# Performance work log

Measured on AMD Instinct MI355X. Metric: run time of the kernel, lower is better.

Reference implementation:

```python
import jax, jax.numpy as jnp
import numpy as np

# ---- module hyperparameters (match init_kwargs) ----
DIM = 512
HEADS = 8
KEY_DIM = 32
ATTN_RATIO = 4
D = ATTN_RATIO * KEY_DIM          # 128, per-head value dim
RES = 28                          # H = W = resolution
B = 64
KS = 5                            # depthwise conv kernel
EPS = 1e-5
SCALE = KEY_DIM ** (-0.5)


def bn(x, p):
    """Inference-mode BatchNorm2d. x: [B,C,H,W], p: [4,C] = (gamma, beta, mean, var)."""
    g, b, m, v = p
    inv = g * jax.lax.rsqrt(v + EPS)
    return x * inv[None, :, None, None] + (b - m * inv)[None, :, None, None]


def conv1x1(x, w):
    """1x1 conv as channel GEMM. x: [B,C,H,W], w: [O,C] -> [B,O,H,W]."""
    return jnp.einsum('oc,bchw->bohw', w, x)


def setup_inputs() -> dict:
    key = jax.random.key(0)
    ks = jax.random.split(key, 12)

    def bnp(k, c):
        k1, k2, k3, k4 = jax.random.split(k, 4)
        return jnp.stack([
            jax.random.uniform(k1, (c,), minval=0.5, maxval=1.5),   # gamma
            jax.random.normal(k2, (c,)) * 0.1,                       # beta
            jax.random.normal(k3, (c,)) * 0.1,                       # running mean
            jax.random.uniform(k4, (c,), minval=0.5, maxval=1.5),   # running var
        ])

    x = jax.random.normal(ks[0], (B, DIM, RES, RES), dtype=jnp.float32)
    qk_w = jax.random.normal(ks[1], (DIM // 2, DIM)) * 0.05
    qk_bn = bnp(ks[2], DIM // 2)
    dws_w = jax.random.normal(ks[3], (DIM // 4, 1, KS, KS)) * 0.05   # depthwise OIHW, I=1
    dws_bn = bnp(ks[4], DIM // 4)
    vs_w = jax.random.normal(ks[5], (HEADS, D, DIM // HEADS)) * 0.05
    vs_bn = jnp.stack([bnp(jax.random.fold_in(ks[6], i), D) for i in range(HEADS)])
    proj_w = jax.random.normal(ks[7], (DIM, D * HEADS)) * 0.05
    proj_bn = bnp(ks[8], DIM)
    # relative-position bias tables over offsets 0..RES-1 (offset -> its own index)
    bias_h = jax.random.normal(ks[9], (1, RES)) * 0.02
    bias_w = jax.random.normal(ks[10], (1, RES)) * 0.02
    bias_idx = jnp.asarray(np.abs(np.arange(RES)[:, None] - np.arange(RES)[None, :]), jnp.int32)
    return dict(x=x, qk_w=qk_w, qk_bn=qk_bn, dws_w=dws_w, dws_bn=dws_bn,
                vs_w=vs_w, vs_bn=vs_bn, proj_w=proj_w, proj_bn=proj_bn,
                bias_h=bias_h, bias_w=bias_w, bias_idx=bias_idx)


def reference(x, qk_w, qk_bn, dws_w, dws_bn, vs_w, vs_bn, proj_w, proj_bn,
              bias_h, bias_w, bias_idx):
    # gathered relative-position biases, [RES, RES]
    ab_h = bias_h[0][bias_idx]
    ab_w = bias_w[0][bias_idx]

    feat = bn(conv1x1(x, qk_w), qk_bn)            # [B, DIM/2, H, W]
    q, k = jnp.split(feat, 2, axis=1)             # each [B, DIM/4, H, W]
    q = bn(jax.lax.conv_general_dilated(
        q, dws_w, (1, 1), 'SAME',
        dimension_numbers=('NCHW', 'OIHW', 'NCHW'),
        feature_group_count=DIM // 4), dws_bn)

    qr_w = q.transpose(0, 2, 3, 1)                # [B, H, W, C4]
    kr_w = k.transpose(0, 2, 3, 1)
    attn_w = jax.nn.softmax(
        jnp.einsum('bhqc,bhkc->bhqk', qr_w, kr_w) * SCALE + ab_w, axis=-1)  # [B,H,W,W]

    qr_h = qr_w.transpose(0, 2, 1, 3)             # [B, W, H, C4]
    kr_h = kr_w.transpose(0, 2, 1, 3)
    attn_h = jax.nn.softmax(
        jnp.einsum('bwqc,bwkc->bwqk', qr_h, kr_h) * SCALE + ab_h, axis=-1)  # [B,W,H,H]

    feats_in = jnp.split(x, HEADS, axis=1)        # each [B, DIM/HEADS, H, W]
    feats_out = []
    feat = feats_in[0]
    for i in range(HEADS):                        # sequential cascade over heads
        if i > 0:
            feat = feat + feats_in[i]
        v = bn(conv1x1(feat, vs_w[i]), vs_bn[i]).transpose(0, 2, 3, 1)  # [B,H,W,D]
        v = jnp.einsum('bhqk,bhkd->bhqd', attn_w, v)                    # row attention
        v = v.transpose(0, 2, 1, 3)                                     # [B,W,H,D]
        f = jnp.einsum('bwqk,bwkd->bwqd', attn_h, v)                    # col attention
        feats_out.append(f.transpose(0, 3, 2, 1))                       # [B,D,H,W]

    out = jnp.concatenate(feats_out, axis=1)      # [B, D*HEADS, H, W]
    out = bn(conv1x1(jax.nn.relu(out), proj_w), proj_bn)                # [B,DIM,H,W]
    return out
```

## Files before the change

kernel.cpp:

```cpp
#include <hip/hip_runtime.h>
#include <hip/hip_fp16.h>

#define NB 64
#define NSP 784
#define CDIM 512
#define CQK 256
#define C4 128
#define NHEADS 8
#define CCAT 1024
#define BN_EPS 1e-5f
#define ATT_SCALE 0.17677669529663687f

using half8_t = __attribute__((ext_vector_type(8))) _Float16;
using half4_t = __attribute__((ext_vector_type(4))) _Float16;
using half2_t = __attribute__((ext_vector_type(2))) _Float16;
using f32x4_t = __attribute__((ext_vector_type(4))) float;

__device__ __forceinline__ void bn_coef(const float* bn, int cout, int o, float& inv, float& add) {
    float g = bn[o], be = bn[cout + o], m = bn[2 * cout + o], v = bn[3 * cout + o];
    inv = g * rsqrtf(v + BN_EPS);
    add = be - m * inv;
}

__device__ __forceinline__ float fdot2(half2_t a, half2_t b, float c) {
#if __has_builtin(__builtin_amdgcn_fdot2)
    return __builtin_amdgcn_fdot2(a, b, c, false);
#else
    return c + (float)a[0] * (float)b[0] + (float)a[1] * (float)b[1];
#endif
}

__device__ __forceinline__ void gload16(const void* g, void* l) {
    __builtin_amdgcn_global_load_lds(
        (const __attribute__((address_space(1))) void*)g,
        (__attribute__((address_space(3))) void*)l, 16, 0, 0);
}

__global__ __launch_bounds__(256)
void transpose_x_kernel(const float* __restrict__ x, _Float16* __restrict__ xt)
{
    __shared__ _Float16 t[32 * 786];
    const int b = blockIdx.y, c0 = blockIdx.x * 32;
    const float* src = x + ((long)b * CDIM + c0) * NSP;
    for (int i = threadIdx.x; i < 32 * NSP; i += 256) {
        const int c = i / NSP, sp = i - c * NSP;
        t[c * 786 + sp] = (_Float16)src[i];
    }
    __syncthreads();
    _Float16* dst = xt + (long)b * NSP * CDIM + c0;
    for (int sp = threadIdx.x; sp < NSP; sp += 256) {
        half8_t* d8 = (half8_t*)(dst + (long)sp * CDIM);
#pragma unroll
        for (int q = 0; q < 4; ++q) {
            half8_t v;
#pragma unroll
            for (int j = 0; j < 8; ++j) v[j] = t[(q * 8 + j) * 786 + sp];
            d8[q] = v;
        }
    }
}

__global__ __launch_bounds__(256)
void convert_w_kernel(const float* __restrict__ qk, const float* __restrict__ vs,
                      const float* __restrict__ pj, _Float16* __restrict__ dst)
{
    const int e = (blockIdx.x * 256 + threadIdx.x) * 4;
    const float* src; int off; _Float16* d;
    if (e < 131072)      { src = qk; off = e;          d = dst; }
    else if (e < 196608) { src = vs; off = e - 131072; d = dst + 131072; }
    else                 { src = pj; off = e - 196608; d = dst + 196608; }
    const float4 v = *(const float4*)(src + off);
    half4_t h; h[0] = (_Float16)v.x; h[1] = (_Float16)v.y; h[2] = (_Float16)v.z; h[3] = (_Float16)v.w;
    *(half4_t*)(d + off) = h;
}

template<int CIN, int NT, bool OUT_T>
__global__ __launch_bounds__(256)
void mfma_gemm_kernel(const _Float16* __restrict__ inH, const _Float16* __restrict__ wA,
                      const float* __restrict__ bnp, void* __restrict__ outp, int cout)
{
    __shared__ _Float16 As[8192];
    __shared__ _Float16 Bs[8192];
    const int tid = threadIdx.x;
    const int lane = tid & 63;
    const int wv = tid >> 6;
    const int wm = wv >> 1, wn = wv & 1;
    const int grp = gridDim.x >> 3;
    const int tile = (blockIdx.x & 7) * grp + (blockIdx.x >> 3);
    const int oBase = (tile % NT) * 128;
    const int colBase = (tile / NT) * 128;

    f32x4_t acc[4][4];
#pragma unroll
    for (int i = 0; i < 4; ++i)
#pragma unroll
        for (int j = 0; j < 4; ++j) acc[i][j] = (f32x4_t){0.f, 0.f, 0.f, 0.f};

    for (int k0 = 0; k0 < CIN; k0 += 64) {
        if (k0) __syncthreads();
#pragma unroll
        for (int it = 0; it < 4; ++it) {
            const int s = it * 256 + tid;
            const int sidx = s >> 3;
            const int skg = (s & 7) ^ (sidx & 7);
            gload16(wA + (long)(oBase + sidx) * CIN + k0 + skg * 8, As + s * 8);
            gload16(inH + (long)(colBase + sidx) * CIN + k0 + skg * 8, Bs + s * 8);
        }
        __syncthreads();
#pragma unroll
        for (int ks = 0; ks < 2; ++ks) {
            const int kq = ks * 4 + (lane >> 4);
            half8_t a[4], b[4];
#pragma unroll
            for (int mf = 0; mf < 4; ++mf) {
                const int idx = wm * 64 + mf * 16 + (lane & 15);
                a[mf] = *(const half8_t*)(As + (idx * 8 + (kq ^ (idx & 7))) * 8);
            }
#pragma unroll
            for (int nf = 0; nf < 4; ++nf) {
                const int idx = wn * 64 + nf * 16 + (lane & 15);
                b[nf] = *(const half8_t*)(Bs + (idx * 8 + (kq ^ (idx & 7))) * 8);
            }
#pragma unroll
            for (int mf = 0; mf < 4; ++mf)
#pragma unroll
                for (int nf = 0; nf < 4; ++nf)
                    acc[mf][nf] = __builtin_amdgcn_mfma_f32_16x16x32_f16(a[mf], b[nf], acc[mf][nf], 0, 0, 0);
        }
    }

    const int rbase = wm * 64 + (lane >> 4) * 4;
    const int cbase = colBase + wn * 64 + (lane & 15);
#pragma unroll
    for (int mf = 0; mf < 4; ++mf) {
        const int o0 = oBase + rbase + mf * 16;
        float inv[4], add[4];
#pragma unroll
        for (int j = 0; j < 4; ++j) bn_coef(bnp, cout, o0 + j, inv[j], add[j]);
#pragma unroll
        for (int nf = 0; nf < 4; ++nf) {
            const int col = cbase + nf * 16;
            if constexpr (OUT_T) {
                _Float16* dst = (_Float16*)outp + (long)col * cout + o0;
                half4_t v;
#pragma unroll
                for (int j = 0; j < 4; ++j) v[j] = (_Float16)(acc[mf][nf][j] * inv[j] + add[j]);
                *(half4_t*)dst = v;
            } else {
                const int bb = col / NSP, sp = col - bb * NSP;
                float* dst = (float*)outp + ((long)bb * cout + o0) * NSP + sp;
#pragma unroll
                for (int j = 0; j < 4; ++j) dst[(long)j * NSP] = acc[mf][nf][j] * inv[j] + add[j];
            }
        }
    }
}

__global__ __launch_bounds__(256)
void vall_kernel(const _Float16* __restrict__ xt, const _Float16* __restrict__ vsw,
                 const float* __restrict__ vsbn, _Float16* __restrict__ concat_t)
{
    __shared__ _Float16 As[8192];
    __shared__ _Float16 Bs[8192];
    const int tid = threadIdx.x, lane = tid & 63;
    const int wv = tid >> 6, wm = wv >> 1, wn = wv & 1;
    const int colBase = blockIdx.x * 128;

    float bacc[4][8];
#pragma unroll
    for (int it = 0; it < 4; ++it)
#pragma unroll
        for (int j = 0; j < 8; ++j) bacc[it][j] = 0.f;

    for (int head = 0; head < NHEADS; ++head) {
        if (head) __syncthreads();
#pragma unroll
        for (int it = 0; it < 4; ++it) {
            const int c = it * 256 + tid;
            const int kg = c & 7, idx = c >> 3;
            const half8_t xv = *(const half8_t*)(xt + (long)(colBase + idx) * CDIM + head * 64 + kg * 8);
            half8_t bv;
#pragma unroll
            for (int j = 0; j < 8; ++j) { bacc[it][j] += (float)xv[j]; bv[j] = (_Float16)bacc[it][j]; }
            *(half8_t*)(Bs + (idx * 8 + (kg ^ (idx & 7))) * 8) = bv;
            const int skg = kg ^ (idx & 7);
            gload16(vsw + (long)head * (C4 * 64) + idx * 64 + skg * 8, As + c * 8);
        }
        __syncthreads();

        f32x4_t acc[4][4];
#pragma unroll
        for (int i = 0; i < 4; ++i)
#pragma unroll
            for (int j = 0; j < 4; ++j) acc[i][j] = (f32x4_t){0.f, 0.f, 0.f, 0.f};
#pragma unroll
        for (int ks = 0; ks < 2; ++ks) {
            const int kq = ks * 4 + (lane >> 4);
            half8_t a[4], b[4];
#pragma unroll
            for (int mf = 0; mf < 4; ++mf) {
                const int idx = wm * 64 + mf * 16 + (lane & 15);
                a[mf] = *(const half8_t*)(As + (idx * 8 + (kq ^ (idx & 7))) * 8);
            }
#pragma unroll
            for (int nf = 0; nf < 4; ++nf) {
                const int idx = wn * 64 + nf * 16 + (lane & 15);
                b[nf] = *(const half8_t*)(Bs + (idx * 8 + (kq ^ (idx & 7))) * 8);
            }
#pragma unroll
            for (int mf = 0; mf < 4; ++mf)
#pragma unroll
                for (int nf = 0; nf < 4; ++nf)
                    acc[mf][nf] = __builtin_amdgcn_mfma_f32_16x16x32_f16(a[mf], b[nf], acc[mf][nf], 0, 0, 0);
        }

        const int rbase = wm * 64 + (lane >> 4) * 4;
        const int cbase = colBase + wn * 64 + (lane & 15);
        const float* bnh = vsbn + head * 4 * C4;
#pragma unroll
        for (int mf = 0; mf < 4; ++mf) {
            const int o0 = rbase + mf * 16;
            float inv[4], add[4];
#pragma unroll
            for (int j = 0; j < 4; ++j) bn_coef(bnh, C4, o0 + j, inv[j], add[j]);
#pragma unroll
            for (int nf = 0; nf < 4; ++nf) {
                const int col = cbase + nf * 16;
                _Float16* dst = concat_t + (long)col * CCAT + head * C4 + o0;
                half4_t v;
#pragma unroll
                for (int j = 0; j < 4; ++j) v[j] = (_Float16)(acc[mf][nf][j] * inv[j] + add[j]);
                *(half4_t*)dst = v;
            }
        }
    }
}

__global__ __launch_bounds__(256)
void dwconv_t_kernel(const _Float16* __restrict__ feat_t, const float* __restrict__ dww,
                     const float* __restrict__ dwbn, _Float16* __restrict__ qdw_t)
{
    const int h = blockIdx.x, b = blockIdx.y, ch0 = blockIdx.z * 64;
    __shared__ _Float16 rows[5][32][64];
    for (int i = threadIdx.x; i < 5 * 32 * 64; i += 256) {
        const int dy = i / (32 * 64);
        const int rem = i - dy * (32 * 64);
        const int iw = rem >> 6, c = rem & 63;
        const int ih = h + dy - 2, w = iw - 2;
        _Float16 v = (_Float16)0.f;
        if (ih >= 0 && ih < 28 && w >= 0 && w < 28)
            v = feat_t[((long)b * NSP + ih * 28 + w) * CQK + ch0 + c];
        rows[dy][iw][c] = v;
    }
    const int pr = threadIdx.x & 31;
    const int c2 = pr * 2;
    float wr0[25], wr1[25];
#pragma unroll
    for (int q = 0; q < 25; ++q) {
        wr0[q] = dww[(ch0 + c2) * 25 + q];
        wr1[q] = dww[(ch0 + c2 + 1) * 25 + q];
    }
    float inv0, add0, inv1, add1;
    bn_coef(dwbn, C4, ch0 + c2, inv0, add0);
    bn_coef(dwbn, C4, ch0 + c2 + 1, inv1, add1);
    __syncthreads();
    for (int l = threadIdx.x; l < 28 * 32; l += 256) {
        const int w = l >> 5;
        float a0 = 0.f, a1 = 0.f;
#pragma unroll
        for (int dy = 0; dy < 5; ++dy)
#pragma unroll
            for (int dx = 0; dx < 5; ++dx) {
                const half2_t v2 = *(const half2_t*)(&rows[dy][w + dx][c2]);
                a0 += wr0[dy * 5 + dx] * (float)v2[0];
                a1 += wr1[dy * 5 + dx] * (float)v2[1];
            }
        half2_t o2; o2[0] = (_Float16)(a0 * inv0 + add0); o2[1] = (_Float16)(a1 * inv1 + add1);
        *(half2_t*)(qdw_t + ((long)b * NSP + h * 28 + w) * C4 + ch0 + c2) = o2;
    }
}

template<bool ROWMODE>
__global__ __launch_bounds__(256)
void attn_map_kernel(const _Float16* __restrict__ qdw_t, const _Float16* __restrict__ feat_t,
                     const float* __restrict__ biasv, _Float16* __restrict__ attn_out)
{
    const int fix = blockIdx.x, b = blockIdx.y;
    __shared__ _Float16 Qs[28][136];
    __shared__ _Float16 Ks[28][136];
    __shared__ float S[28][28];
    __shared__ float bsh[28];
    if (threadIdx.x < 28) bsh[threadIdx.x] = biasv[threadIdx.x];
    for (int l = threadIdx.x; l < 28 * 16; l += 256) {
        const int p = l >> 4, c8 = (l & 15) * 8;
        const int sp = ROWMODE ? (fix * 28 + p) : (p * 28 + fix);
        *(half8_t*)(&Qs[p][c8]) = *(const half8_t*)(qdw_t + ((long)b * NSP + sp) * C4 + c8);
        *(half8_t*)(&Ks[p][c8]) = *(const half8_t*)(feat_t + ((long)b * NSP + sp) * CQK + 128 + c8);
    }
    __syncthreads();
    for (int e = threadIdx.x; e < 784; e += 256) {
        const int qp = e / 28, kp = e - (e / 28) * 28;
        float acc = 0.f;
        const half2_t* qv = (const half2_t*)&Qs[qp][0];
        const half2_t* kv = (const half2_t*)&Ks[kp][0];
#pragma unroll
        for (int c = 0; c < 64; ++c) acc = fdot2(qv[c], kv[c], acc);
        const int dd = qp - kp;
        S[qp][kp] = acc * ATT_SCALE + bsh[dd < 0 ? -dd : dd];
    }
    __syncthreads();
    const int r = threadIdx.x >> 3, g = threadIdx.x & 7;
    if (r < 28) {
        float mx = -1e30f;
#pragma unroll
        for (int j = 0; j < 4; ++j) { const int k = g + j * 8; if (k < 28) mx = fmaxf(mx, S[r][k]); }
        mx = fmaxf(mx, __shfl_xor(mx, 1));
        mx = fmaxf(mx, __shfl_xor(mx, 2));
        mx = fmaxf(mx, __shfl_xor(mx, 4));
        float e4[4], sum = 0.f;
#pragma unroll
        for (int j = 0; j < 4; ++j) {
            const int k = g + j * 8;
            e4[j] = (k < 28) ? __expf(S[r][k] - mx) : 0.f;
            sum += e4[j];
        }
        sum += __shfl_xor(sum, 1);
        sum += __shfl_xor(sum, 2);
        sum += __shfl_xor(sum, 4);
        const float rinv = 1.f / sum;
#pragma unroll
        for (int j = 0; j < 4; ++j) { const int k = g + j * 8; if (k < 28) S[r][k] = e4[j] * rinv; }
    }
    __syncthreads();
    _Float16* dst = attn_out + ((long)b * 28 + fix) * 1024;
    for (int i = threadIdx.x; i < 1024; i += 256) {
        const int q = i >> 5, k = i & 31;
        dst[i] = (q < 28 && k < 28) ? (_Float16)S[q][k] : (_Float16)0.f;
    }
}

__global__ __launch_bounds__(512)
void fused_stage_kernel(_Float16* __restrict__ concat_t,
                        const _Float16* __restrict__ attw,
                        const _Float16* __restrict__ atth)
{
    const int wgid = ((int)blockIdx.x & 7) * ((int)gridDim.x >> 3) + ((int)blockIdx.x >> 3);
    const int b = wgid >> 6, dq = wgid & 63;
    __shared__ _Float16 V[16 * 906];
    __shared__ _Float16 M1[28 * 17 * 42];
    const int tid = threadIdx.x, lane = tid & 63, wv = tid >> 6;
    const int kg = lane >> 4, lr = lane & 15;

    _Float16* cbase = concat_t + (long)b * NSP * CCAT + dq * 16;

    for (int p = tid; p < 16 * 28 * 4; p += 512) {
        const int d = p / 112, rem = p - d * 112;
        V[d * 906 + (rem >> 2) * 32 + 28 + (rem & 3)] = (_Float16)0.f;
    }
    for (int p = tid; p < 28 * 16 * 4; p += 512) {
        const int w = p >> 6, rem = p & 63;
        M1[(w * 17 + (rem >> 2)) * 42 + 28 + (rem & 3)] = (_Float16)0.f;
    }
    for (int t = tid; t < 1568; t += 512) {
        const int sp = t >> 1, c0 = (t & 1) * 8;
        const int r = sp / 28, j = sp - r * 28;
        const half8_t v = *(const half8_t*)(cbase + (long)sp * CCAT + c0);
#pragma unroll
        for (int q = 0; q < 8; ++q) V[(c0 + q) * 906 + r * 32 + j] = v[q];
    }
    __syncthreads();

    for (int r = wv; r < 28; r += 8) {
        const _Float16* bw = attw + ((long)b * 28 + r) * 1024;
        const half8_t a0 = *(const half8_t*)(V + lr * 906 + r * 32 + kg * 8);
        const half8_t b0 = *(const half8_t*)(bw + lr * 32 + kg * 8);
        const half8_t b1 = *(const half8_t*)(bw + (16 + lr) * 32 + kg * 8);
        f32x4_t acc0 = (f32x4_t){0.f, 0.f, 0.f, 0.f};
        f32x4_t acc1 = (f32x4_t){0.f, 0.f, 0.f, 0.f};
        acc0 = __builtin_amdgcn_mfma_f32_16x16x32_f16(a0, b0, acc0, 0, 0, 0);
        acc1 = __builtin_amdgcn_mfma_f32_16x16x32_f16(a0, b1, acc1, 0, 0, 0);
#pragma unroll
        for (int q = 0; q < 4; ++q) {
            const int d = kg * 4 + q;
            M1[(lr * 17 + d) * 42 + r] = (_Float16)acc0[q];
            if (16 + lr < 28) M1[((16 + lr) * 17 + d) * 42 + r] = (_Float16)acc1[q];
        }
    }
    __syncthreads();

    for (int w = wv; w < 28; w += 8) {
        const _Float16* bh = atth + ((long)b * 28 + w) * 1024;
        const half8_t a0 = *(const half8_t*)(M1 + (w * 17 + lr) * 42 + kg * 8);
        const half8_t b0 = *(const half8_t*)(bh + lr * 32 + kg * 8);
        const half8_t b1 = *(const half8_t*)(bh + (16 + lr) * 32 + kg * 8);
        f32x4_t acc0 = (f32x4_t){0.f, 0.f, 0.f, 0.f};
        f32x4_t acc1 = (f32x4_t){0.f, 0.f, 0.f, 0.f};
        acc0 = __builtin_amdgcn_mfma_f32_16x16x32_f16(a0, b0, acc0, 0, 0, 0);
        acc1 = __builtin_amdgcn_mfma_f32_16x16x32_f16(a0, b1, acc1, 0, 0, 0);
        const int d0 = kg * 4;
        {
            const int hh = lr;
            const int sp = hh * 28 + w;
            half4_t v;
#pragma unroll
            for (int q = 0; q < 4; ++q) v[q] = (_Float16)fmaxf(acc0[q], 0.f);
            *(half4_t*)(cbase + (long)sp * CCAT + d0) = v;
        }
        if (16 + lr < 28) {
            const int hh = 16 + lr;
            const int sp = hh * 28 + w;
            half4_t v;
#pragma unroll
            for (int q = 0; q < 4; ++q) v[q] = (_Float16)fmaxf(acc1[q], 0.f);
            *(half4_t*)(cbase + (long)sp * CCAT + d0) = v;
        }
    }
}

extern "C" void kernel_launch(void* const* d_in, const int* in_sizes, int n_in,
                              void* d_out, int out_size, void* d_ws, size_t ws_size,
                              hipStream_t stream)
{
    const float* x        = (const float*)d_in[0];
    const float* qk_w     = (const float*)d_in[1];
    const float* qk_bn    = (const float*)d_in[2];
    const float* dws_w    = (const float*)d_in[3];
    const float* dws_bn   = (const float*)d_in[4];
    const float* vs_w     = (const float*)d_in[5];
    const float* vs_bn    = (const float*)d_in[6];
    const float* proj_w   = (const float*)d_in[7];
    const float* proj_bn  = (const float*)d_in[8];
    const float* bias_h   = (const float*)d_in[9];
    const float* bias_w   = (const float*)d_in[10];

    char* ob = (char*)d_out;
    _Float16* x_t    = (_Float16*)ob;
    _Float16* attw_p = (_Float16*)(ob + 51380224);
    _Float16* atth_p = (_Float16*)(ob + 55050240);
    _Float16* feat_t = (_Float16*)(ob + 58720256);
    _Float16* qdw_t  = (_Float16*)(ob + 84410368);

    _Float16* concat_t = (_Float16*)d_ws;
    _Float16* w_h      = (_Float16*)((char*)d_ws + 102760448);
    _Float16* qk_w_h   = w_h;
    _Float16* vs_w_h   = w_h + 131072;
    _Float16* proj_w_h = w_h + 196608;

    transpose_x_kernel<<<dim3(16, NB), 256, 0, stream>>>(x, x_t);
    convert_w_kernel<<<704, 256, 0, stream>>>(qk_w, vs_w, proj_w, w_h);

    mfma_gemm_kernel<CDIM, 2, true><<<784, 256, 0, stream>>>(
        x_t, qk_w_h, qk_bn, feat_t, CQK);
    dwconv_t_kernel<<<dim3(28, NB, 2), 256, 0, stream>>>(feat_t, dws_w, dws_bn, qdw_t);
    attn_map_kernel<true><<<dim3(28, NB), 256, 0, stream>>>(qdw_t, feat_t, bias_w, attw_p);
    attn_map_kernel<false><<<dim3(28, NB), 256, 0, stream>>>(qdw_t, feat_t, bias_h, atth_p);

    vall_kernel<<<392, 256, 0, stream>>>(x_t, vs_w_h, vs_bn, concat_t);

    fused_stage_kernel<<<4096, 512, 0, stream>>>(concat_t, attw_p, atth_p);

    mfma_gemm_kernel<CCAT, 4, false><<<1568, 256, 0, stream>>>(
        concat_t, proj_w_h, proj_bn, (float*)d_out, CDIM);
}
```

Before: 371.6 us.

## Store V channel-major so fused stage reads rows directly without LDS staging

vall_kernel now writes V in a [B, C, spatial] layout into the output buffer. This lets fused_stage_kernel load MFMA A-fragments straight from global memory instead of transposing through an LDS tile, which removes that LDS buffer and one barrier. Results go to a separate concat_out buffer rather than in place, and workspace and output buffers are reassigned to fit. The cost is that the vall epilogue now does strided scalar stores instead of half4 stores, and the direct fragment loads are unaligned 16-byte global reads.

```diff
diff --git a/kernel.cpp b/kernel.cpp
--- a/kernel.cpp
+++ b/kernel.cpp
@@ -158,7 +158,7 @@
 
 __global__ __launch_bounds__(256)
 void vall_kernel(const _Float16* __restrict__ xt, const _Float16* __restrict__ vsw,
-                 const float* __restrict__ vsbn, _Float16* __restrict__ concat_t)
+                 const float* __restrict__ vsbn, _Float16* __restrict__ concat_v)
 {
     __shared__ _Float16 As[8192];
     __shared__ _Float16 Bs[8192];
@@ -226,11 +226,11 @@
 #pragma unroll
             for (int nf = 0; nf < 4; ++nf) {
                 const int col = cbase + nf * 16;
-                _Float16* dst = concat_t + (long)col * CCAT + head * C4 + o0;
-                half4_t v;
-#pragma unroll
-                for (int j = 0; j < 4; ++j) v[j] = (_Float16)(acc[mf][nf][j] * inv[j] + add[j]);
-                *(half4_t*)dst = v;
+                const int bb = col / NSP, sp = col - bb * NSP;
+                _Float16* dst = concat_v + ((long)bb * CCAT + head * C4 + o0) * NSP + sp;
+#pragma unroll
+                for (int j = 0; j < 4; ++j)
+                    dst[(long)j * NSP] = (_Float16)(acc[mf][nf][j] * inv[j] + add[j]);
             }
         }
     }
@@ -340,39 +340,33 @@
 }
 
 __global__ __launch_bounds__(512)
-void fused_stage_kernel(_Float16* __restrict__ concat_t,
+void fused_stage_kernel(const _Float16* __restrict__ concat_v,
                         const _Float16* __restrict__ attw,
-                        const _Float16* __restrict__ atth)
+                        const _Float16* __restrict__ atth,
+                        _Float16* __restrict__ concat_out)
 {
     const int wgid = ((int)blockIdx.x & 7) * ((int)gridDim.x >> 3) + ((int)blockIdx.x >> 3);
     const int b = wgid >> 6, dq = wgid & 63;
-    __shared__ _Float16 V[16 * 906];
     __shared__ _Float16 M1[28 * 17 * 42];
     const int tid = threadIdx.x, lane = tid & 63, wv = tid >> 6;
     const int kg = lane >> 4, lr = lane & 15;
 
-    _Float16* cbase = concat_t + (long)b * NSP * CCAT + dq * 16;
-
-    for (int p = tid; p < 16 * 28 * 4; p += 512) {
-        const int d = p / 112, rem = p - d * 112;
-        V[d * 906 + (rem >> 2) * 32 + 28 + (rem & 3)] = (_Float16)0.f;
-    }
-    for (int p = tid; p < 28 * 16 * 4; p += 512) {
-        const int w = p >> 6, rem = p & 63;
-        M1[(w * 17 + (rem >> 2)) * 42 + 28 + (rem & 3)] = (_Float16)0.f;
-    }
-    for (int t = tid; t < 1568; t += 512) {
-        const int sp = t >> 1, c0 = (t & 1) * 8;
-        const int r = sp / 28, j = sp - r * 28;
-        const half8_t v = *(const half8_t*)(cbase + (long)sp * CCAT + c0);
-#pragma unroll
-        for (int q = 0; q < 8; ++q) V[(c0 + q) * 906 + r * 32 + j] = v[q];
-    }
-    __syncthreads();
+    const _Float16* vbase = concat_v + ((long)b * CCAT + dq * 16) * NSP;
+
+    for (int p = tid; p < 28 * 17 * 4; p += 512)
+        M1[(p >> 2) * 42 + 28 + (p & 3)] = (_Float16)0.f;
 
     for (int r = wv; r < 28; r += 8) {
         const _Float16* bw = attw + ((long)b * 28 + r) * 1024;
-        const half8_t a0 = *(const half8_t*)(V + lr * 906 + r * 32 + kg * 8);
+        const long vrow = (long)lr * NSP + r * 28;
+        half8_t a0;
+        if (kg < 3) {
+            a0 = *(const half8_t*)(vbase + vrow + kg * 8);
+        } else {
+            const half4_t lo = *(const half4_t*)(vbase + vrow + 24);
+            a0 = (half8_t){lo[0], lo[1], lo[2], lo[3],
+                           (_Float16)0.f, (_Float16)0.f, (_Float16)0.f, (_Float16)0.f};
+        }
         const half8_t b0 = *(const half8_t*)(bw + lr * 32 + kg * 8);
         const half8_t b1 = *(const half8_t*)(bw + (16 + lr) * 32 + kg * 8);
         f32x4_t acc0 = (f32x4_t){0.f, 0.f, 0.f, 0.f};
@@ -388,6 +382,7 @@
     }
     __syncthreads();
 
+    _Float16* obase = concat_out + (long)b * NSP * CCAT + dq * 16;
     for (int w = wv; w < 28; w += 8) {
         const _Float16* bh = atth + ((long)b * 28 + w) * 1024;
         const half8_t a0 = *(const half8_t*)(M1 + (w * 17 + lr) * 42 + kg * 8);
@@ -399,20 +394,18 @@
         acc1 = __builtin_amdgcn_mfma_f32_16x16x32_f16(a0, b1, acc1, 0, 0, 0);
         const int d0 = kg * 4;
         {
-            const int hh = lr;
-            const int sp = hh * 28 + w;
+            const int sp = lr * 28 + w;
             half4_t v;
 #pragma unroll
             for (int q = 0; q < 4; ++q) v[q] = (_Float16)fmaxf(acc0[q], 0.f);
-            *(half4_t*)(cbase + (long)sp * CCAT + d0) = v;
+            *(half4_t*)(obase + (long)sp * CCAT + d0) = v;
         }
         if (16 + lr < 28) {
-            const int hh = 16 + lr;
-            const int sp = hh * 28 + w;
+            const int sp = (16 + lr) * 28 + w;
             half4_t v;
 #pragma unroll
             for (int q = 0; q < 4; ++q) v[q] = (_Float16)fmaxf(acc1[q], 0.f);
-            *(half4_t*)(cbase + (long)sp * CCAT + d0) = v;
+            *(half4_t*)(obase + (long)sp * CCAT + d0) = v;
         }
     }
 }
@@ -433,18 +426,20 @@
     const float* bias_h   = (const float*)d_in[9];
     const float* bias_w   = (const float*)d_in[10];
 
+    char* wsb = (char*)d_ws;
+    _Float16* concat_out = (_Float16*)wsb;
+    _Float16* x_t        = (_Float16*)wsb;
+    _Float16* attw_p     = (_Float16*)(wsb + 102760448);
+    _Float16* atth_p     = (_Float16*)(wsb + 106430464);
+    _Float16* w_h        = (_Float16*)(wsb + 110100480);
+    _Float16* qk_w_h     = w_h;
+    _Float16* vs_w_h     = w_h + 131072;
+    _Float16* proj_w_h   = w_h + 196608;
+
     char* ob = (char*)d_out;
-    _Float16* x_t    = (_Float16*)ob;
-    _Float16* attw_p = (_Float16*)(ob + 51380224);
-    _Float16* atth_p = (_Float16*)(ob + 55050240);
-    _Float16* feat_t = (_Float16*)(ob + 58720256);
-    _Float16* qdw_t  = (_Float16*)(ob + 84410368);
-
-    _Float16* concat_t = (_Float16*)d_ws;
-    _Float16* w_h      = (_Float16*)((char*)d_ws + 102760448);
-    _Float16* qk_w_h   = w_h;
-    _Float16* vs_w_h   = w_h + 131072;
-    _Float16* proj_w_h = w_h + 196608;
+    _Float16* feat_t   = (_Float16*)ob;
+    _Float16* qdw_t    = (_Float16*)(ob + 25690112);
+    _Float16* concat_v = (_Float16*)ob;
 
     transpose_x_kernel<<<dim3(16, NB), 256, 0, stream>>>(x, x_t);
     convert_w_kernel<<<704, 256, 0, stream>>>(qk_w, vs_w, proj_w, w_h);
@@ -455,10 +450,10 @@
     attn_map_kernel<true><<<dim3(28, NB), 256, 0, stream>>>(qdw_t, feat_t, bias_w, attw_p);
     attn_map_kernel<false><<<dim3(28, NB), 256, 0, stream>>>(qdw_t, feat_t, bias_h, atth_p);
 
-    vall_kernel<<<392, 256, 0, stream>>>(x_t, vs_w_h, vs_bn, concat_t);
-
-    fused_stage_kernel<<<4096, 512, 0, stream>>>(concat_t, attw_p, atth_p);
+    vall_kernel<<<392, 256, 0, stream>>>(x_t, vs_w_h, vs_bn, concat_v);
+
+    fused_stage_kernel<<<4096, 512, 0, stream>>>(concat_v, attw_p, atth_p, concat_out);
 
     mfma_gemm_kernel<CCAT, 4, false><<<1568, 256, 0, stream>>>(
-        concat_t, proj_w_h, proj_bn, (float*)d_out, CDIM);
-}
+        concat_out, proj_w_h, proj_bn, (float*)d_out, CDIM);
+}
```

Result: faster. 354.3 us (-4.6%).
